# Kernel optimization log

Measured on AMD Instinct MI355X. Metric: run time of the kernel, lower is better.

## Reference

```python
import jax, jax.numpy as jnp
import numpy as np

B, N, H = 4096, 64, 16  # batch, board side, max hints per row/col
FALLBACK_SIZE = 12


def setup_inputs() -> dict:
    key = jax.random.key(0)
    k1, k2, k3, k4 = jax.random.split(key, 4)
    grid = jax.random.normal(k1, (B, 1, N, N), dtype=jnp.float32)
    hints = jax.random.randint(k2, (B, 2, N, H), 0, 3).astype(jnp.float32)
    w_g = jax.random.normal(k3, (1, N, N), dtype=jnp.float32)
    w_h = jax.random.normal(k4, (2, N, H), dtype=jnp.float32)
    return {"grid": grid, "hints": hints, "w_g": w_g, "w_h": w_h}


def reference(grid, hints, w_g, w_h):
    # neural energy: simple linear energy head standing in for self.model(grid, hints)
    neural_energy = jnp.mean(
        jnp.einsum('bchw,chw->b', grid, w_g)
        + jnp.einsum('bkhm,khm->b', hints, w_h)
    )

    n = grid.shape[2]
    sg = jax.nn.sigmoid(grid[:, 0] * 3.0)          # [B,N,N] soft grid
    row_hints = hints[:, 0]                         # [B,N,H]
    col_hints = hints[:, 1]                         # [B,N,H]

    # per-sample puzzle size: last row/col index that has any hint, +1; else 12
    idx = jnp.arange(n)
    row_has = row_hints.sum(-1) > 0                 # [B,N]
    col_has = col_hints.sum(-1) > 0                 # [B,N]
    last_r = jnp.max(jnp.where(row_has, idx, -1), axis=1)
    last_c = jnp.max(jnp.where(col_has, idx, -1), axis=1)
    size = jnp.where((last_r >= 0) & (last_c >= 0),
                     jnp.maximum(last_r, last_c) + 1,
                     FALLBACK_SIZE)                 # [B]
    m = (idx[None, :] < size[:, None]).astype(grid.dtype)  # [B,N] validity mask
    sz = size.astype(grid.dtype)

    # logic energy: masked row/col sum MSE (sum reduction / size), mean over batch * 10
    row_target = row_hints.sum(-1)                  # [B,N]
    col_target = col_hints.sum(-1)                  # [B,N]
    actual_rows = jnp.einsum('bij,bj->bi', sg, m)   # sum over cols j < size
    actual_cols = jnp.einsum('bij,bi->bj', sg, m)   # sum over rows i < size
    row_err = jnp.sum((actual_rows - row_target) ** 2 * m, axis=-1) / sz
    col_err = jnp.sum((actual_cols - col_target) ** 2 * m, axis=-1) / sz
    logic_energy = jnp.mean(row_err + col_err) * 10.0

    # binary energy: mean of grid^2 over the size x size sub-board, mean over batch * 0.1
    m2 = m[:, :, None] * m[:, None, :]              # [B,N,N]
    bin_per = jnp.sum(grid[:, 0] ** 2 * m2, axis=(1, 2)) / (sz * sz)
    binary_energy = jnp.mean(bin_per) * 0.1

    return neural_energy + logic_energy + binary_energy
```

## Files before the change

kernel.cpp:

```cpp
#include <hip/hip_runtime.h>

#define B_TOT 4096
#define NWS 64

__global__ void zero_ws_kernel(float* ws) {
    ws[threadIdx.x] = 0.f;
}

__global__ __launch_bounds__(256) void energy_kernel(
    const float* __restrict__ grid,
    const float* __restrict__ hints,
    const float* __restrict__ w_g,
    const float* __restrict__ w_h,
    float* __restrict__ ws)
{
    const int b   = blockIdx.x;
    const int tid = threadIdx.x;

    __shared__ float s[64 * 65];
    __shared__ float target[2][64];
    __shared__ int   s_size;
    __shared__ float red[4];

    const float* hb = hints + (size_t)b * 2048;
    float4 h0 = *(const float4*)(hb + 8 * tid);
    float4 h1 = *(const float4*)(hb + 8 * tid + 4);
    float4 w0 = *(const float4*)(w_h + 8 * tid);
    float4 w1 = *(const float4*)(w_h + 8 * tid + 4);
    float dot_h = h0.x * w0.x + h0.y * w0.y + h0.z * w0.z + h0.w * w0.w
                + h1.x * w1.x + h1.y * w1.y + h1.z * w1.z + h1.w * w1.w;
    float hsum = h0.x + h0.y + h0.z + h0.w + h1.x + h1.y + h1.z + h1.w;
    hsum += __shfl_xor(hsum, 1);
    if ((tid & 1) == 0) {
        target[tid >> 7][(tid >> 1) & 63] = hsum;
    }
    __syncthreads();

    if (tid < 64) {
        unsigned long long mr = __ballot(target[0][tid] > 0.f);
        unsigned long long mc = __ballot(target[1][tid] > 0.f);
        if (tid == 0) {
            int last_r = mr ? (63 - __builtin_clzll(mr)) : -1;
            int last_c = mc ? (63 - __builtin_clzll(mc)) : -1;
            s_size = (last_r >= 0 && last_c >= 0) ? (max(last_r, last_c) + 1)
                                                  : 12;
        }
    }
    __syncthreads();
    const int   size = s_size;
    const float sz   = (float)size;

    const float* gb = grid + (size_t)b * 4096;
    float neural = dot_h;
    float binp   = 0.f;
    #pragma unroll
    for (int k = 0; k < 4; ++k) {
        int q = tid + 256 * k;
        float4 g = *(const float4*)(gb + 4 * q);
        float4 w = *(const float4*)(w_g + 4 * q);
        neural += g.x * w.x + g.y * w.y + g.z * w.z + g.w * w.w;
        int row = q >> 4;
        int c0  = (q & 15) * 4;
        if (row < size) {
            float bs = 0.f;
            if (c0 + 0 < size) bs += g.x * g.x;
            if (c0 + 1 < size) bs += g.y * g.y;
            if (c0 + 2 < size) bs += g.z * g.z;
            if (c0 + 3 < size) bs += g.w * g.w;
            binp += bs;
        }
        float* sp = s + row * 65 + c0;
        sp[0] = 1.f / (1.f + __expf(-3.f * g.x));
        sp[1] = 1.f / (1.f + __expf(-3.f * g.y));
        sp[2] = 1.f / (1.f + __expf(-3.f * g.z));
        sp[3] = 1.f / (1.f + __expf(-3.f * g.w));
    }
    __syncthreads();

    float errp = 0.f;
    {
        int r = tid >> 2, qq = tid & 3;
        float acc = 0.f;
        #pragma unroll
        for (int x = 0; x < 16; ++x) {
            int j = 16 * qq + x;
            acc += (j < size) ? s[r * 65 + j] : 0.f;
        }
        acc += __shfl_xor(acc, 1);
        acc += __shfl_xor(acc, 2);
        if (qq == 0 && r < size) {
            float d = acc - target[0][r];
            errp += d * d;
        }
    }
    {
        int c = tid >> 2, qq = tid & 3;
        float acc = 0.f;
        #pragma unroll
        for (int x = 0; x < 16; ++x) {
            int i = 16 * qq + x;
            acc += (i < size) ? s[i * 65 + c] : 0.f;
        }
        acc += __shfl_xor(acc, 1);
        acc += __shfl_xor(acc, 2);
        if (qq == 0 && c < size) {
            float d = acc - target[1][c];
            errp += d * d;
        }
    }

    float v = neural + errp * (10.f / sz) + binp * (0.1f / (sz * sz));
    #pragma unroll
    for (int off = 1; off < 64; off <<= 1) v += __shfl_xor(v, off);
    if ((tid & 63) == 0) red[tid >> 6] = v;
    __syncthreads();
    if (tid == 0) {
        float tot = (red[0] + red[1] + red[2] + red[3]) * (1.f / (float)B_TOT);
        atomicAdd(&ws[b & (NWS - 1)], tot);
    }
}

__global__ void final_reduce_kernel(const float* __restrict__ ws,
                                    float* __restrict__ out) {
    float v = ws[threadIdx.x];
    #pragma unroll
    for (int off = 1; off < 64; off <<= 1) v += __shfl_xor(v, off);
    if (threadIdx.x == 0) out[0] = v;
}

extern "C" void kernel_launch(void* const* d_in, const int* in_sizes, int n_in,
                              void* d_out, int out_size, void* d_ws, size_t ws_size,
                              hipStream_t stream) {
    const float* grid_p  = (const float*)d_in[0];
    const float* hints_p = (const float*)d_in[1];
    const float* w_g     = (const float*)d_in[2];
    const float* w_h     = (const float*)d_in[3];
    float* out = (float*)d_out;
    float* ws  = (float*)d_ws;

    zero_ws_kernel<<<1, NWS, 0, stream>>>(ws);
    energy_kernel<<<B_TOT, 256, 0, stream>>>(grid_p, hints_p, w_g, w_h, ws);
    final_reduce_kernel<<<1, 64, 0, stream>>>(ws, out);
}
```

Before: 132.3 us.

## Compute row/col sums in registers via shuffles, drop shared tile and atomics

The 64x65 shared-memory tile of sigmoid values is removed. Row sums are now reduced with 16-lane shuffles, and column sums are accumulated per thread, reduced across lanes, then combined through a small shared array. All grid and weight loads are issued up front. Per-block results go to a per-batch workspace slot instead of atomics, so the zero-init kernel is gone and a wider final reduce kernel is used. This removes shared-memory traffic, a barrier and a launch, at the cost of more registers and a larger final reduction.

```diff
diff --git a/kernel.cpp b/kernel.cpp
--- a/kernel.cpp
+++ b/kernel.cpp
@@ -1,11 +1,6 @@
 #include <hip/hip_runtime.h>
 
 #define B_TOT 4096
-#define NWS 64
-
-__global__ void zero_ws_kernel(float* ws) {
-    ws[threadIdx.x] = 0.f;
-}
 
 __global__ __launch_bounds__(256) void energy_kernel(
     const float* __restrict__ grid,
@@ -14,26 +9,37 @@
     const float* __restrict__ w_h,
     float* __restrict__ ws)
 {
-    const int b   = blockIdx.x;
-    const int tid = threadIdx.x;
+    const int b    = blockIdx.x;
+    const int tid  = threadIdx.x;
+    const int lane = tid & 63;
+    const int wv   = tid >> 6;
 
-    __shared__ float s[64 * 65];
-    __shared__ float target[2][64];
-    __shared__ int   s_size;
-    __shared__ float red[4];
+    __shared__ float  target[2][64];
+    __shared__ float4 colp4[4][16];
+    __shared__ int    s_size;
+    __shared__ float  red[4];
 
     const float* hb = hints + (size_t)b * 2048;
+    const float* gb = grid  + (size_t)b * 4096;
+
     float4 h0 = *(const float4*)(hb + 8 * tid);
     float4 h1 = *(const float4*)(hb + 8 * tid + 4);
-    float4 w0 = *(const float4*)(w_h + 8 * tid);
-    float4 w1 = *(const float4*)(w_h + 8 * tid + 4);
-    float dot_h = h0.x * w0.x + h0.y * w0.y + h0.z * w0.z + h0.w * w0.w
-                + h1.x * w1.x + h1.y * w1.y + h1.z * w1.z + h1.w * w1.w;
+    float4 g0 = *(const float4*)(gb + 4 * tid);
+    float4 g1 = *(const float4*)(gb + 4 * tid + 1024);
+    float4 g2 = *(const float4*)(gb + 4 * tid + 2048);
+    float4 g3 = *(const float4*)(gb + 4 * tid + 3072);
+    float4 wh0 = *(const float4*)(w_h + 8 * tid);
+    float4 wh1 = *(const float4*)(w_h + 8 * tid + 4);
+    float4 wg0 = *(const float4*)(w_g + 4 * tid);
+    float4 wg1 = *(const float4*)(w_g + 4 * tid + 1024);
+    float4 wg2 = *(const float4*)(w_g + 4 * tid + 2048);
+    float4 wg3 = *(const float4*)(w_g + 4 * tid + 3072);
+
+    float neural = h0.x * wh0.x + h0.y * wh0.y + h0.z * wh0.z + h0.w * wh0.w
+                 + h1.x * wh1.x + h1.y * wh1.y + h1.z * wh1.z + h1.w * wh1.w;
     float hsum = h0.x + h0.y + h0.z + h0.w + h1.x + h1.y + h1.z + h1.w;
     hsum += __shfl_xor(hsum, 1);
-    if ((tid & 1) == 0) {
-        target[tid >> 7][(tid >> 1) & 63] = hsum;
-    }
+    if ((tid & 1) == 0) target[tid >> 7][(tid >> 1) & 63] = hsum;
     __syncthreads();
 
     if (tid < 64) {
@@ -42,69 +48,68 @@
         if (tid == 0) {
             int last_r = mr ? (63 - __builtin_clzll(mr)) : -1;
             int last_c = mc ? (63 - __builtin_clzll(mc)) : -1;
-            s_size = (last_r >= 0 && last_c >= 0) ? (max(last_r, last_c) + 1)
-                                                  : 12;
+            s_size = (last_r >= 0 && last_c >= 0) ? (max(last_r, last_c) + 1) : 12;
         }
     }
     __syncthreads();
     const int   size = s_size;
     const float sz   = (float)size;
 
-    const float* gb = grid + (size_t)b * 4096;
-    float neural = dot_h;
-    float binp   = 0.f;
+    const int c0   = (tid & 15) * 4;
+    const int rbase = tid >> 4;
+    const float mx = (c0 + 0 < size) ? 1.f : 0.f;
+    const float my = (c0 + 1 < size) ? 1.f : 0.f;
+    const float mz = (c0 + 2 < size) ? 1.f : 0.f;
+    const float mw = (c0 + 3 < size) ? 1.f : 0.f;
+
+    float binp = 0.f;
+    float errp = 0.f;
+    float4 cacc = {0.f, 0.f, 0.f, 0.f};
+
+    float4 gk[4] = {g0, g1, g2, g3};
+    float4 wk[4] = {wg0, wg1, wg2, wg3};
     #pragma unroll
     for (int k = 0; k < 4; ++k) {
-        int q = tid + 256 * k;
-        float4 g = *(const float4*)(gb + 4 * q);
-        float4 w = *(const float4*)(w_g + 4 * q);
+        float4 g = gk[k];
+        float4 w = wk[k];
         neural += g.x * w.x + g.y * w.y + g.z * w.z + g.w * w.w;
-        int row = q >> 4;
-        int c0  = (q & 15) * 4;
-        if (row < size) {
-            float bs = 0.f;
-            if (c0 + 0 < size) bs += g.x * g.x;
-            if (c0 + 1 < size) bs += g.y * g.y;
-            if (c0 + 2 < size) bs += g.z * g.z;
-            if (c0 + 3 < size) bs += g.w * g.w;
-            binp += bs;
+        int   row  = rbase + 16 * k;
+        float rmask = (row < size) ? 1.f : 0.f;
+        binp += rmask * (mx * g.x * g.x + my * g.y * g.y + mz * g.z * g.z + mw * g.w * g.w);
+
+        float sx = 1.f / (1.f + __expf(-3.f * g.x));
+        float sy = 1.f / (1.f + __expf(-3.f * g.y));
+        float sz_ = 1.f / (1.f + __expf(-3.f * g.z));
+        float sw = 1.f / (1.f + __expf(-3.f * g.w));
+
+        float rs = mx * sx + my * sy + mz * sz_ + mw * sw;
+        rs += __shfl_xor(rs, 1);
+        rs += __shfl_xor(rs, 2);
+        rs += __shfl_xor(rs, 4);
+        rs += __shfl_xor(rs, 8);
+        if ((lane & 15) == 0 && row < size) {
+            float d = rs - target[0][row];
+            errp += d * d;
         }
-        float* sp = s + row * 65 + c0;
-        sp[0] = 1.f / (1.f + __expf(-3.f * g.x));
-        sp[1] = 1.f / (1.f + __expf(-3.f * g.y));
-        sp[2] = 1.f / (1.f + __expf(-3.f * g.z));
-        sp[3] = 1.f / (1.f + __expf(-3.f * g.w));
+
+        cacc.x += rmask * sx;
+        cacc.y += rmask * sy;
+        cacc.z += rmask * sz_;
+        cacc.w += rmask * sw;
     }
+
+    cacc.x += __shfl_xor(cacc.x, 16); cacc.x += __shfl_xor(cacc.x, 32);
+    cacc.y += __shfl_xor(cacc.y, 16); cacc.y += __shfl_xor(cacc.y, 32);
+    cacc.z += __shfl_xor(cacc.z, 16); cacc.z += __shfl_xor(cacc.z, 32);
+    cacc.w += __shfl_xor(cacc.w, 16); cacc.w += __shfl_xor(cacc.w, 32);
+    if (lane < 16) colp4[wv][lane] = cacc;
     __syncthreads();
 
-    float errp = 0.f;
-    {
-        int r = tid >> 2, qq = tid & 3;
-        float acc = 0.f;
-        #pragma unroll
-        for (int x = 0; x < 16; ++x) {
-            int j = 16 * qq + x;
-            acc += (j < size) ? s[r * 65 + j] : 0.f;
-        }
-        acc += __shfl_xor(acc, 1);
-        acc += __shfl_xor(acc, 2);
-        if (qq == 0 && r < size) {
-            float d = acc - target[0][r];
-            errp += d * d;
-        }
-    }
-    {
-        int c = tid >> 2, qq = tid & 3;
-        float acc = 0.f;
-        #pragma unroll
-        for (int x = 0; x < 16; ++x) {
-            int i = 16 * qq + x;
-            acc += (i < size) ? s[i * 65 + c] : 0.f;
-        }
-        acc += __shfl_xor(acc, 1);
-        acc += __shfl_xor(acc, 2);
-        if (qq == 0 && c < size) {
-            float d = acc - target[1][c];
+    if (tid < 64) {
+        const float* cp = (const float*)colp4;
+        float csum = cp[tid] + cp[64 + tid] + cp[128 + tid] + cp[192 + tid];
+        if (tid < size) {
+            float d = csum - target[1][tid];
             errp += d * d;
         }
     }
@@ -112,20 +117,30 @@
     float v = neural + errp * (10.f / sz) + binp * (0.1f / (sz * sz));
     #pragma unroll
     for (int off = 1; off < 64; off <<= 1) v += __shfl_xor(v, off);
-    if ((tid & 63) == 0) red[tid >> 6] = v;
+    if (lane == 0) red[wv] = v;
     __syncthreads();
-    if (tid == 0) {
-        float tot = (red[0] + red[1] + red[2] + red[3]) * (1.f / (float)B_TOT);
-        atomicAdd(&ws[b & (NWS - 1)], tot);
-    }
+    if (tid == 0) ws[b] = red[0] + red[1] + red[2] + red[3];
 }
 
-__global__ void final_reduce_kernel(const float* __restrict__ ws,
-                                    float* __restrict__ out) {
-    float v = ws[threadIdx.x];
+__global__ __launch_bounds__(1024) void final_reduce_kernel(
+    const float* __restrict__ ws, float* __restrict__ out)
+{
+    const int tid = threadIdx.x;
+    float4 v4 = ((const float4*)ws)[tid];
+    float v = v4.x + v4.y + v4.z + v4.w;
     #pragma unroll
     for (int off = 1; off < 64; off <<= 1) v += __shfl_xor(v, off);
-    if (threadIdx.x == 0) out[0] = v;
+    __shared__ float r[16];
+    if ((tid & 63) == 0) r[tid >> 6] = v;
+    __syncthreads();
+    if (tid < 16) {
+        float t = r[tid];
+        t += __shfl_xor(t, 1);
+        t += __shfl_xor(t, 2);
+        t += __shfl_xor(t, 4);
+        t += __shfl_xor(t, 8);
+        if (tid == 0) out[0] = t * (1.f / (float)B_TOT);
+    }
 }
 
 extern "C" void kernel_launch(void* const* d_in, const int* in_sizes, int n_in,
@@ -138,7 +153,6 @@
     float* out = (float*)d_out;
     float* ws  = (float*)d_ws;
 
-    zero_ws_kernel<<<1, NWS, 0, stream>>>(ws);
     energy_kernel<<<B_TOT, 256, 0, stream>>>(grid_p, hints_p, w_g, w_h, ws);
-    final_reduce_kernel<<<1, 64, 0, stream>>>(ws, out);
+    final_reduce_kernel<<<1, 1024, 0, stream>>>(ws, out);
 }
```

After: 120.0 us. -9.3%, faster.
